# Kernel optimization log

Measured on AMD Instinct MI355X. Metric: run time of the kernel, lower is better.

The kernel has to match this reference:

```python
import jax, jax.numpy as jnp
import numpy as np
from jax import lax

C1, C2 = 64, 128
B, H2, W2 = 16, 64, 64
EPS = 1e-5


def conv2d(x, w, b, pad):
    y = lax.conv_general_dilated(x, w, (1, 1), [(pad, pad), (pad, pad)],
                                 dimension_numbers=('NCHW', 'OIHW', 'NCHW'))
    return y + b[None, :, None, None]


def batchnorm(x, g, be):
    # training-mode BN (batch statistics), matching torch nn.BatchNorm2d default
    m = jnp.mean(x, axis=(0, 2, 3), keepdims=True)
    v = jnp.var(x, axis=(0, 2, 3), keepdims=True)
    return (x - m) * jax.lax.rsqrt(v + EPS) * g[None, :, None, None] + be[None, :, None, None]


def up2_bilinear_ac(x):
    # bilinear upsample x2 with align_corners=True (nn.UpsamplingBilinear2d)
    b, c, h, w = x.shape
    yy = jnp.arange(2 * h, dtype=x.dtype) * ((h - 1) / (2 * h - 1))
    xx = jnp.arange(2 * w, dtype=x.dtype) * ((w - 1) / (2 * w - 1))
    y0 = jnp.floor(yy).astype(jnp.int32); y1 = jnp.minimum(y0 + 1, h - 1)
    x0 = jnp.floor(xx).astype(jnp.int32); x1 = jnp.minimum(x0 + 1, w - 1)
    wy = (yy - y0.astype(x.dtype))
    wx = (xx - x0.astype(x.dtype))
    rows = x[:, :, y0, :] * (1 - wy)[:, None] + x[:, :, y1, :] * wy[:, None]
    return rows[:, :, :, x0] * (1 - wx) + rows[:, :, :, x1] * wx


def dilate(x, k):
    # grayscale morphological dilation with kxk ones kernel == sliding-window max
    return lax.reduce_window(x, -jnp.inf, lax.max, (1, 1, k, k), (1, 1, 1, 1), 'SAME')


def pixel_shuffle2(x):
    b, c, h, w = x.shape
    x = x.reshape(b, c // 4, 2, 2, h, w)
    return x.transpose(0, 1, 4, 2, 5, 3).reshape(b, c // 4, 2 * h, 2 * w)


def setup_inputs() -> dict:
    key = jax.random.key(0)
    ks = jax.random.split(key, 16)
    s = 0.05
    d = {
        'cur_x': jax.random.normal(ks[0], (B, C1, 2 * H2, 2 * W2), jnp.float32),
        'dep_x': jax.random.normal(ks[1], (B, C2, H2, W2), jnp.float32),
        'in_map': jax.random.normal(ks[2], (B, 1, H2, W2), jnp.float32),
        'up_w': jax.random.normal(ks[3], (4 * C1, C2, 3, 3), jnp.float32) * s,
        'up_b': jnp.zeros((4 * C1,), jnp.float32),
        'up_g': jnp.ones((4 * C1,), jnp.float32),
        'up_be': jnp.zeros((4 * C1,), jnp.float32),
        'conv2_w': jax.random.normal(ks[4], (C1, C1, 3, 3), jnp.float32) * s,
        'conv2_b': jnp.zeros((C1,), jnp.float32),
        'beta': jnp.ones((1,), jnp.float32),
        'd1_w': jax.random.normal(ks[5], (C1, C1, 3, 3), jnp.float32) * s,
        'd1_b': jnp.zeros((C1,), jnp.float32),
        'd1_g': jnp.ones((C1,), jnp.float32),
        'd1_be': jnp.zeros((C1,), jnp.float32),
        'd2_w': jax.random.normal(ks[6], (C1, C1, 3, 3), jnp.float32) * s,
        'd2_b': jnp.zeros((C1,), jnp.float32),
        'd2_g': jnp.ones((C1,), jnp.float32),
        'd2_be': jnp.zeros((C1,), jnp.float32),
        'd3_w': jax.random.normal(ks[7], (C1, C1, 3, 3), jnp.float32) * s,
        'd3_b': jnp.zeros((C1,), jnp.float32),
        'd3_g': jnp.ones((C1,), jnp.float32),
        'd3_be': jnp.zeros((C1,), jnp.float32),
        'out_w': jax.random.normal(ks[8], (1, C1, 7, 7), jnp.float32) * s,
        'out_b': jnp.zeros((1,), jnp.float32),
    }
    return d


def reference(cur_x, dep_x, in_map, up_w, up_b, up_g, up_be, conv2_w, conv2_b, beta,
              d1_w, d1_b, d1_g, d1_be, d2_w, d2_b, d2_g, d2_be, d3_w, d3_b, d3_g, d3_be,
              out_w, out_b):
    # up: conv(C2 -> 4*C1) + BN + ReLU, then PixelShuffle(2)
    dep = jax.nn.relu(batchnorm(conv2d(dep_x, up_w, up_b, 1), up_g, up_be))
    dep = pixel_shuffle2(dep)                       # [B, C1, H, W]
    imap = jax.nn.sigmoid(up2_bilinear_ac(in_map))  # [B, 1, H, W]
    # focus_background: dilated(map) - map (increase_input_map is identity, sf=1)
    increase_map = dilate(imap, 3) - imap
    b_feature = cur_x * increase_map
    fn = conv2d(b_feature, conv2_w, conv2_b, 1)
    r = jax.nn.relu(batchnorm(conv2d(dep + beta * fn, d1_w, d1_b, 1), d1_g, d1_be))
    r = jax.nn.relu(batchnorm(conv2d(r, d2_w, d2_b, 1), d2_g, d2_be))
    r = jax.nn.relu(batchnorm(conv2d(r, d3_w, d3_b, 1), d3_g, d3_be))
    output_map = conv2d(r, out_w, out_b, 3)
    return (r, output_map)
```

## Files before the change

### kernel.cpp

```cpp
#include <hip/hip_runtime.h>
#include <hip/hip_bf16.h>

using bf16 = __hip_bfloat16;
typedef __attribute__((ext_vector_type(8))) short bfrag;
typedef __attribute__((ext_vector_type(4))) float ffrag;

__device__ __forceinline__ float b2f(bf16 v) { return __bfloat162float(v); }
__device__ __forceinline__ float ldin(const void* p, int i, int isbf) {
    return isbf ? b2f(((const bf16*)p)[i]) : ((const float*)p)[i];
}
__device__ __forceinline__ void split2(float v, unsigned short& h, unsigned short& l) {
    bf16 hb = __float2bfloat16(v);
    h = __bfloat16_as_ushort(hb);
    l = __bfloat16_as_ushort(__float2bfloat16(v - __bfloat162float(hb)));
}

__global__ void detect_kernel(const unsigned* __restrict__ x, int* __restrict__ flag)
{
    int tid = threadIdx.x;
    int cnt = 0;
    for (int i = tid; i < 256; i += 64) {
        unsigned e = (x[i] >> 7) & 0xFFu;
        cnt += (e >= 110u && e <= 135u) ? 1 : 0;
    }
#pragma unroll
    for (int off = 32; off > 0; off >>= 1) cnt += __shfl_down(cnt, off, 64);
    if (tid == 0) *flag = (cnt >= 128) ? 1 : 0;
}

__global__ void zero_accum_kernel(float* __restrict__ a)
{
    for (int i = threadIdx.x; i < 896; i += 256) a[i] = 0.f;
}

template<int CIN, int COUT>
__global__ __launch_bounds__(256)
void wsplit_kernel(const void* __restrict__ w, unsigned short* __restrict__ whi,
                   unsigned short* __restrict__ wlo, const int* __restrict__ flagp)
{
    constexpr int NCH = CIN / 32, NCOG = COUT / 16;
    constexpr int total = 9 * NCH * NCOG * 512;
    int isbf = *flagp;
    int o = blockIdx.x * 256 + threadIdx.x;
    if (o >= total) return;
    int j = o & 7;
    int l = (o >> 3) & 63;
    int fb = o >> 9;
    int cg = fb % NCOG;
    int t2 = fb / NCOG;
    int ch = t2 % NCH;
    int tap = t2 / NCH;
    int co = cg * 16 + (l & 15);
    int ci = ch * 32 + (l >> 4) * 8 + j;
    float v = ldin(w, (co * CIN + ci) * 9 + tap, isbf);
    unsigned short h, lo2;
    split2(v, h, lo2);
    whi[o] = h;
    wlo[o] = lo2;
}

__global__ __launch_bounds__(256)
void dep_nhwc_kernel(const void* __restrict__ in, unsigned short* __restrict__ outp,
                     const int* __restrict__ flagp)
{
    __shared__ unsigned short s_h[64][65];
    __shared__ unsigned short s_l[64][65];
    const int isbf = *flagp;
    const int pb = blockIdx.x, cb = blockIdx.y, b = blockIdx.z;
    for (int i = threadIdx.x; i < 4096; i += 256) {
        int ci = i >> 6, pi = i & 63;
        float v = ldin(in, ((b * 128 + cb * 64 + ci) << 12) + (pb << 6) + pi, isbf);
        unsigned short h, l;
        split2(v, h, l);
        s_h[ci][pi] = h;
        if (!isbf) s_l[ci][pi] = l;
    }
    __syncthreads();
    for (int i = threadIdx.x; i < 4096; i += 256) {
        int ci = i & 63, pi = i >> 6;
        size_t o = ((size_t)(b * 4096 + pb * 64 + pi) << 7) + cb * 64 + ci;
        outp[o] = s_h[ci][pi];
        if (!isbf) outp[8388608 + o] = s_l[ci][pi];
    }
}

template<int CIN, int COUT, int H, int W, int ROWS, int WCO, int MODE,
         bool SMAP, bool EPI, bool BNIN, bool STATS, int MINW>
__global__ __launch_bounds__(256, MINW)
void conv3_mfma(const void* __restrict__ in,
                const unsigned short* __restrict__ whi,
                const unsigned short* __restrict__ wlo,
                const void* __restrict__ bias,
                const float* __restrict__ imapF,
                const float* __restrict__ dep,
                const void* __restrict__ betap,
                const float* __restrict__ accum,
                const void* __restrict__ bng, const void* __restrict__ bnbe,
                float* __restrict__ out, const int* __restrict__ flagp,
                float* __restrict__ sacc, int statC)
{
    constexpr int NCH  = CIN / 32;
    constexpr int NCOG = COUT / 16;
    constexpr int NCT  = W / 64;
    constexpr int W2h  = 66;
    constexpr int NP   = (ROWS + 2) * W2h;
    constexpr int NPs  = NP + 1;
    constexpr int NE   = 4 * NP;
    constexpr int NF   = (64 / WCO) / 16;
    constexpr int STCO = 64 / WCO;
    constexpr size_t PLANE = (size_t)16 * H * W * CIN;

    __shared__ int4 s_hi[4 * NPs];
    __shared__ int4 s_lo[4 * NPs];
    __shared__ float s_ss[BNIN ? 128 : 1];
    __shared__ float s_sm[SMAP ? NP : 1];
    __shared__ float s_st[STATS ? 2 : 1][4][STCO];

    const int isbf = *flagp;
    const bool uselo = !(isbf && (MODE == 2 || (MODE == 1 && !SMAP)));
    const int tid  = threadIdx.x;
    const int r0   = (blockIdx.x / NCT) * ROWS;
    const int x0   = (blockIdx.x % NCT) * 64;
    const int bimg = r0 / H;
    const int y0im = bimg * H;
    const int coB  = blockIdx.y;

    if (BNIN) {
        if (tid < CIN) {
            const float n = (float)(16 * H * W);
            float S = accum[tid], S2 = accum[CIN + tid];
            float m = S / n;
            float var = fmaxf(S2 / n - m * m, 0.f);
            float scv = ldin(bng, tid, isbf) * rsqrtf(var + 1e-5f);
            s_ss[2 * tid]     = scv;
            s_ss[2 * tid + 1] = ldin(bnbe, tid, isbf) - m * scv;
        }
    }
    if (SMAP) {
        const float* ip = imapF + ((size_t)bimg << 14);
        for (int i = tid; i < NP; i += 256) {
            int rr = i / W2h, cc = i - rr * W2h;
            int gy = r0 - 1 + rr, gx = x0 - 1 + cc;
            float sm = 0.f;
            if (gy >= y0im && gy < y0im + H && (unsigned)gx < (unsigned)W) {
                int y = gy - y0im;
                float ctr = ip[(y << 7) + gx];
                float mx = ctr;
#pragma unroll
                for (int dy = -1; dy <= 1; dy++) {
                    int yy = y + dy;
                    if ((unsigned)yy < 128u) {
#pragma unroll
                        for (int dx = -1; dx <= 1; dx++) {
                            int xx = gx + dx;
                            if ((unsigned)xx < 128u) mx = fmaxf(mx, ip[(yy << 7) + xx]);
                        }
                    }
                }
                sm = mx - ctr;
            }
            s_sm[i] = sm;
        }
    }

    const int lane = tid & 63;
    const int wv = tid >> 6;
    const int wpx = wv / WCO, wco = wv % WCO;
    const int lx = lane & 15;
    const int gq = lane >> 4;

    ffrag acc[4][NF];
#pragma unroll
    for (int mf = 0; mf < 4; mf++)
#pragma unroll
        for (int nf = 0; nf < NF; nf++) acc[mf][nf] = ffrag{0.f, 0.f, 0.f, 0.f};

    for (int ch = 0; ch < NCH; ch++) {
        const int c0 = ch * 32;
        __syncthreads();
        for (int e = tid; e < NE; e += 256) {
            int gg, pixin;
            if (MODE == 1) { gg = e / NP; pixin = e - gg * NP; }
            else           { gg = e & 3;  pixin = e >> 2; }
            int rr = pixin / W2h;
            int cc2 = pixin - rr * W2h;
            int gy = r0 - 1 + rr;
            int gx = x0 - 1 + cc2;
            bool ok = (gy >= y0im) && (gy < y0im + H) && ((unsigned)gx < (unsigned)W);
            if (MODE == 2) {
                int4 hv = make_int4(0, 0, 0, 0), lv = make_int4(0, 0, 0, 0);
                if (ok) {
                    size_t eb = (size_t)(gy * W + gx) * CIN + c0 + 8 * gg;
                    hv = *(const int4*)((const unsigned short*)in + eb);
                    if (!isbf) lv = *(const int4*)((const unsigned short*)in + PLANE + eb);
                }
                s_hi[gg * NPs + pixin] = hv;
                if (!isbf) s_lo[gg * NPs + pixin] = lv;
            } else {
                float v[8];
                if (ok) {
                    if (MODE == 1) {
                        int y = gy - y0im;
                        float sm = SMAP ? s_sm[pixin] : 1.f;
#pragma unroll
                        for (int j = 0; j < 8; j++) {
                            int gi = ((bimg * CIN + c0 + 8 * gg + j) * H + y) * W + gx;
                            v[j] = ldin(in, gi, isbf) * sm;
                        }
                    } else {
                        const float* up = (const float*)in +
                            ((size_t)gy * W + gx) * CIN + c0 + 8 * gg;
                        float4 q0 = *(const float4*)up;
                        float4 q1 = *(const float4*)(up + 4);
                        v[0] = q0.x; v[1] = q0.y; v[2] = q0.z; v[3] = q0.w;
                        v[4] = q1.x; v[5] = q1.y; v[6] = q1.z; v[7] = q1.w;
                        if (BNIN) {
#pragma unroll
                            for (int j = 0; j < 8; j++) {
                                int chn = c0 + 8 * gg + j;
                                v[j] = fmaxf(fmaf(v[j], s_ss[2 * chn], s_ss[2 * chn + 1]), 0.f);
                            }
                        }
                    }
                } else {
#pragma unroll
                    for (int j = 0; j < 8; j++) v[j] = 0.f;
                }
                unsigned hp[4], lp[4];
#pragma unroll
                for (int j2 = 0; j2 < 4; j2++) {
                    bf16 h0b = __float2bfloat16(v[2 * j2]);
                    bf16 h1b = __float2bfloat16(v[2 * j2 + 1]);
                    hp[j2] = (unsigned)__bfloat16_as_ushort(h0b) |
                             ((unsigned)__bfloat16_as_ushort(h1b) << 16);
                    if (uselo) {
                        unsigned short l0 = __bfloat16_as_ushort(
                            __float2bfloat16(v[2 * j2] - b2f(h0b)));
                        unsigned short l1 = __bfloat16_as_ushort(
                            __float2bfloat16(v[2 * j2 + 1] - b2f(h1b)));
                        lp[j2] = (unsigned)l0 | ((unsigned)l1 << 16);
                    }
                }
                s_hi[gg * NPs + pixin] = make_int4(hp[0], hp[1], hp[2], hp[3]);
                if (uselo)
                    s_lo[gg * NPs + pixin] = make_int4(lp[0], lp[1], lp[2], lp[3]);
            }
        }
        __syncthreads();
#pragma unroll
        for (int tap = 0; tap < 9; tap++) {
            const int ky = tap / 3, kx = tap % 3;
            bfrag ah[4];
#pragma unroll
            for (int mf = 0; mf < 4; mf++) {
                int p = 64 * wpx + 16 * mf;
                int rI = (p >> 6) + ky;
                int cI = (p & 63) + kx + lx;
                int pix = rI * W2h + cI;
                ah[mf] = ((const bfrag*)s_hi)[gq * NPs + pix];
            }
            bfrag bh[NF];
#pragma unroll
            for (int nf = 0; nf < NF; nf++) {
                int fb = (tap * NCH + ch) * NCOG + coB * 4 + wco * NF + nf;
                bh[nf] = ((const bfrag*)(whi + (size_t)fb * 512))[lane];
            }
#pragma unroll
            for (int nf = 0; nf < NF; nf++)
#pragma unroll
                for (int mf = 0; mf < 4; mf++)
                    acc[mf][nf] = __builtin_amdgcn_mfma_f32_16x16x32_bf16(
                        ah[mf], bh[nf], acc[mf][nf], 0, 0, 0);
            if (uselo) {
                bfrag al[4];
#pragma unroll
                for (int mf = 0; mf < 4; mf++) {
                    int p = 64 * wpx + 16 * mf;
                    int rI = (p >> 6) + ky;
                    int cI = (p & 63) + kx + lx;
                    int pix = rI * W2h + cI;
                    al[mf] = ((const bfrag*)s_lo)[gq * NPs + pix];
                }
#pragma unroll
                for (int nf = 0; nf < NF; nf++)
#pragma unroll
                    for (int mf = 0; mf < 4; mf++)
                        acc[mf][nf] = __builtin_amdgcn_mfma_f32_16x16x32_bf16(
                            al[mf], bh[nf], acc[mf][nf], 0, 0, 0);
            }
            if (!isbf) {
                bfrag ah2[4];
#pragma unroll
                for (int mf = 0; mf < 4; mf++) {
                    int p = 64 * wpx + 16 * mf;
                    int rI = (p >> 6) + ky;
                    int cI = (p & 63) + kx + lx;
                    int pix = rI * W2h + cI;
                    ah2[mf] = ((const bfrag*)s_hi)[gq * NPs + pix];
                }
                bfrag bl[NF];
#pragma unroll
                for (int nf = 0; nf < NF; nf++) {
                    int fb = (tap * NCH + ch) * NCOG + coB * 4 + wco * NF + nf;
                    bl[nf] = ((const bfrag*)(wlo + (size_t)fb * 512))[lane];
                }
#pragma unroll
                for (int nf = 0; nf < NF; nf++)
#pragma unroll
                    for (int mf = 0; mf < 4; mf++)
                        acc[mf][nf] = __builtin_amdgcn_mfma_f32_16x16x32_bf16(
                            ah2[mf], bl[nf], acc[mf][nf], 0, 0, 0);
            }
        }
    }
    const float beta = EPI ? ldin(betap, 0, isbf) : 0.f;
    float sl[NF], s2l[NF];
#pragma unroll
    for (int nf = 0; nf < NF; nf++) { sl[nf] = 0.f; s2l[nf] = 0.f; }
#pragma unroll
    for (int nf = 0; nf < NF; nf++) {
        int co = coB * 64 + wco * STCO + nf * 16 + lx;
        float bi = ldin(bias, co, isbf);
#pragma unroll
        for (int mf = 0; mf < 4; mf++) {
#pragma unroll
            for (int r2 = 0; r2 < 4; r2++) {
                int p = 64 * wpx + 16 * mf + gq * 4 + r2;
                int grow = r0 + (p >> 6);
                int gcol = x0 + (p & 63);
                size_t oi = ((size_t)grow * W + gcol) * COUT + co;
                float vo = acc[mf][nf][r2] + bi;
                if (EPI) vo = dep[oi] + beta * vo;
                out[oi] = vo;
                if (STATS) {
                    sl[nf] += vo;
                    s2l[nf] = fmaf(vo, vo, s2l[nf]);
                }
            }
        }
    }
    if (STATS) {
#pragma unroll
        for (int nf = 0; nf < NF; nf++) {
            float s = sl[nf], q = s2l[nf];
            s += __shfl_xor(s, 16, 64); s += __shfl_xor(s, 32, 64);
            q += __shfl_xor(q, 16, 64); q += __shfl_xor(q, 32, 64);
            if (gq == 0) {
                s_st[0][wv][nf * 16 + lx] = s;
                s_st[1][wv][nf * 16 + lx] = q;
            }
        }
        __syncthreads();
        if (tid < 128) {
            int which = tid >> 6, c = tid & 63;
            float v;
            if (WCO == 1) {
                v = s_st[which][0][c] + s_st[which][1][c] +
                    s_st[which][2][c] + s_st[which][3][c];
            } else {
                int wc = c >> 5, ci = c & 31;
                v = s_st[which][wc][ci] + s_st[which][2 + wc][ci];
            }
            atomicAdd(&sacc[which * statC + coB * 64 + c], v);
        }
    }
}

__global__ __launch_bounds__(256)
void shuffle_bn_nhwc_kernel(const float* __restrict__ u, const float* __restrict__ accum,
                            const void* __restrict__ g, const void* __restrict__ be,
                            float* __restrict__ dep, const int* __restrict__ flagp)
{
    int isbf = *flagp;
    int tid = threadIdx.x;
    int c = tid & 63, ps = tid >> 6;
    float sc[4], sh[4];
#pragma unroll
    for (int q = 0; q < 4; q++) {
        int chn = 4 * c + q;
        float S = accum[chn], S2 = accum[256 + chn];
        const float n = 65536.f;
        float m = S / n;
        float var = fmaxf(S2 / n - m * m, 0.f);
        sc[q] = ldin(g, chn, isbf) * rsqrtf(var + 1e-5f);
        sh[q] = ldin(be, chn, isbf) - m * sc[q];
    }
    for (int sp = blockIdx.x * 4 + ps; sp < 65536; sp += gridDim.x * 4) {
        float4 q4 = *(const float4*)(u + (size_t)sp * 256 + 4 * c);
        float vals[4] = {q4.x, q4.y, q4.z, q4.w};
        int b = sp >> 12, rem = sp & 4095, y2 = rem >> 6, x2 = rem & 63;
#pragma unroll
        for (int dy = 0; dy < 2; dy++)
#pragma unroll
            for (int dx = 0; dx < 2; dx++) {
                int q = 2 * dy + dx;
                float v = fmaxf(fmaf(vals[q], sc[q], sh[q]), 0.f);
                size_t op = (size_t)(b * 128 + 2 * y2 + dy) * 128 + (2 * x2 + dx);
                dep[op * 64 + c] = v;
            }
    }
}

__global__ __launch_bounds__(256)
void imap_kernel(const void* __restrict__ im, float* __restrict__ imap,
                 const int* __restrict__ flagp)
{
    int isbf = *flagp;
    int idx = blockIdx.x * 256 + threadIdx.x;
    int x = idx & 127, y = (idx >> 7) & 127, b = idx >> 14;
    const float s = (float)(63.0 / 127.0);
    float yy = y * s, xx = x * s;
    int y0 = (int)yy, x0 = (int)xx;
    float wy = yy - y0, wx = xx - x0;
    int y1 = min(y0 + 1, 63), x1 = min(x0 + 1, 63);
    int base = b << 12;
    float v00 = ldin(im, base + (y0 << 6) + x0, isbf);
    float v01 = ldin(im, base + (y0 << 6) + x1, isbf);
    float v10 = ldin(im, base + (y1 << 6) + x0, isbf);
    float v11 = ldin(im, base + (y1 << 6) + x1, isbf);
    float r0 = v00 * (1.f - wy) + v10 * wy;
    float r1 = v01 * (1.f - wy) + v11 * wy;
    float v = r0 * (1.f - wx) + r1 * wx;
    imap[idx] = 1.f / (1.f + expf(-v));
}

__global__ __launch_bounds__(256)
void bn_out_kernel(const float* __restrict__ u, const float* __restrict__ accum,
                   const void* __restrict__ g, const void* __restrict__ be,
                   float* __restrict__ r3, void* __restrict__ dout,
                   const int* __restrict__ flagp)
{
    int isbf = *flagp;
    int tid = threadIdx.x;
    int c = tid & 63, ps = tid >> 6;
    float S = accum[c], S2 = accum[64 + c];
    const float n = 262144.f;
    float m = S / n;
    float var = fmaxf(S2 / n - m * m, 0.f);
    float sc = ldin(g, c, isbf) * rsqrtf(var + 1e-5f);
    float sh = ldin(be, c, isbf) - m * sc;
    __shared__ float s[64][65];
    int pix0 = blockIdx.x * 64;
#pragma unroll
    for (int ii = 0; ii < 16; ii++) {
        int p = ps + 4 * ii;
        float v = u[(size_t)(pix0 + p) * 64 + c];
        s[p][c] = fmaxf(fmaf(v, sc, sh), 0.f);
    }
    __syncthreads();
    int x = c;
    int row = pix0 >> 7, col0 = pix0 & 127;
    int b = row >> 7, y = row & 127;
#pragma unroll
    for (int jj = 0; jj < 16; jj++) {
        int cc = ps + 4 * jj;
        float v = s[x][cc];
        size_t oi = (((size_t)(b * 64 + cc)) << 14) + (y << 7) + col0 + x;
        r3[oi] = v;
        if (isbf) ((bf16*)dout)[oi] = __float2bfloat16(v);
        else      ((float*)dout)[oi] = v;
    }
}

__global__ __launch_bounds__(256, 2)
void conv7x7_part_kernel(const float* __restrict__ r, const void* __restrict__ w,
                         float* __restrict__ outP, const int* __restrict__ flagp)
{
    __shared__ float s_in[4][70][22];
    __shared__ float s_w[16][49];
    const int isbf = *flagp;
    int tid = threadIdx.x;
    int tx = tid & 15, ty = tid >> 4;
    int x0 = blockIdx.x * 16, y0 = blockIdx.y * 64;
    int b = blockIdx.z >> 2, g = blockIdx.z & 3;
    for (int i = tid; i < 16 * 49; i += 256) {
        int ci = i / 49, k = i - ci * 49;
        s_w[ci][k] = ldin(w, (g * 16 + ci) * 49 + k, isbf);
    }
    float acc[4] = {0.f, 0.f, 0.f, 0.f};

    for (int c0 = 0; c0 < 16; c0 += 4) {
        __syncthreads();
        for (int i = tid; i < 4 * 70 * 22; i += 256) {
            int ci = i / (70 * 22);
            int rem = i - ci * (70 * 22);
            int rr = rem / 22, cc = rem - rr * 22;
            int gy = y0 + rr - 3, gx = x0 + cc - 3;
            float v = 0.f;
            if ((unsigned)gy < 128u && (unsigned)gx < 128u)
                v = r[((b * 64 + g * 16 + c0 + ci) << 14) + (gy << 7) + gx];
            s_in[ci][rr][cc] = v;
        }
        __syncthreads();
        for (int ci = 0; ci < 4; ci++) {
            float wr[49];
#pragma unroll
            for (int k = 0; k < 49; k++) wr[k] = s_w[c0 + ci][k];
#pragma unroll
            for (int rr = 0; rr < 10; rr++) {
                float row[7];
#pragma unroll
                for (int c = 0; c < 7; c++) row[c] = s_in[ci][4 * ty + rr][tx + c];
#pragma unroll
                for (int oy = 0; oy < 4; oy++) {
                    int ky = rr - oy;
                    if (ky >= 0 && ky <= 6) {
#pragma unroll
                        for (int kx = 0; kx < 7; kx++)
                            acc[oy] = fmaf(row[kx], wr[ky * 7 + kx], acc[oy]);
                    }
                }
            }
        }
    }
#pragma unroll
    for (int oy = 0; oy < 4; oy++) {
        int y = y0 + 4 * ty + oy;
        outP[(g << 18) + (b << 14) + (y << 7) + x0 + tx] = acc[oy];
    }
}

__global__ __launch_bounds__(256)
void finalize_out_kernel(const float* __restrict__ outP, const void* __restrict__ bias,
                         void* __restrict__ outv, const int* __restrict__ flagp)
{
    int isbf = *flagp;
    int i = blockIdx.x * 256 + threadIdx.x;
    float bi = ldin(bias, 0, isbf);
    float v = (outP[i] + outP[i + 262144]) +
              (outP[i + 2 * 262144] + outP[i + 3 * 262144]) + bi;
    int oidx = 16777216 + i;
    if (isbf) ((bf16*)outv)[oidx] = __float2bfloat16(v);
    else      ((float*)outv)[oidx] = v;
}

extern "C" void kernel_launch(void* const* d_in, const int* in_sizes, int n_in,
                              void* d_out, int out_size, void* d_ws, size_t ws_size,
                              hipStream_t stream)
{
    (void)in_sizes; (void)n_in; (void)out_size; (void)ws_size;

    const void* cur_x   = d_in[0];
    const void* dep_x   = d_in[1];
    const void* in_map  = d_in[2];
    const void* up_w    = d_in[3];
    const void* up_b    = d_in[4];
    const void* up_g    = d_in[5];
    const void* up_be   = d_in[6];
    const void* conv2_w = d_in[7];
    const void* conv2_b = d_in[8];
    const void* beta    = d_in[9];
    const void* d1_w = d_in[10];
    const void* d1_b = d_in[11];
    const void* d1_g = d_in[12];
    const void* d1_be = d_in[13];
    const void* d2_w = d_in[14];
    const void* d2_b = d_in[15];
    const void* d2_g = d_in[16];
    const void* d2_be = d_in[17];
    const void* d3_w = d_in[18];
    const void* d3_b = d_in[19];
    const void* d3_g = d_in[20];
    const void* d3_be = d_in[21];
    const void* out_w = d_in[22];
    const void* out_b = d_in[23];

    char* ws = (char*)d_ws;
    float* W0    = (float*)ws;
    float* W1    = (float*)(ws + 67108864);
    float* accum = (float*)(ws + 134217728);
    int*   flag  = (int*)(ws + 134221824);
    float* a0 = accum;
    float* a1 = accum + 512;
    float* a2 = accum + 640;
    float* a3 = accum + 768;

    char* sc = (char*)d_out;
    unsigned short* whi1  = (unsigned short*)sc;
    unsigned short* wlo1  = whi1 + 294912;
    unsigned short* whi2  = wlo1 + 294912;
    unsigned short* wlo2  = whi2 + 36864;
    unsigned short* whiD1 = wlo2 + 36864;
    unsigned short* wloD1 = whiD1 + 36864;
    unsigned short* whiD2 = wloD1 + 36864;
    unsigned short* wloD2 = whiD2 + 36864;
    unsigned short* whiD3 = wloD2 + 36864;
    unsigned short* wloD3 = whiD3 + 36864;
    float* imapF = (float*)(sc + 1769472);

    detect_kernel<<<1, 64, 0, stream>>>((const unsigned*)cur_x, flag);
    zero_accum_kernel<<<1, 256, 0, stream>>>(accum);
    wsplit_kernel<128, 256><<<1152, 256, 0, stream>>>(up_w, whi1, wlo1, flag);
    wsplit_kernel<64, 64><<<144, 256, 0, stream>>>(conv2_w, whi2, wlo2, flag);
    wsplit_kernel<64, 64><<<144, 256, 0, stream>>>(d1_w, whiD1, wloD1, flag);
    wsplit_kernel<64, 64><<<144, 256, 0, stream>>>(d2_w, whiD2, wloD2, flag);
    wsplit_kernel<64, 64><<<144, 256, 0, stream>>>(d3_w, whiD3, wloD3, flag);
    dep_nhwc_kernel<<<dim3(64, 2, 16), 256, 0, stream>>>(
        dep_x, (unsigned short*)W1, flag);

    conv3_mfma<128, 256, 64, 64, 4, 1, 2, false, false, false, true, 3>
        <<<dim3(256, 4), 256, 0, stream>>>((const void*)W1, whi1, wlo1, up_b,
            nullptr, nullptr, nullptr, nullptr, nullptr, nullptr, W0, flag, a0, 256);
    imap_kernel<<<1024, 256, 0, stream>>>(in_map, imapF, flag);
    shuffle_bn_nhwc_kernel<<<2048, 256, 0, stream>>>(W0, a0, up_g, up_be, W1, flag);
    conv3_mfma<64, 64, 128, 128, 2, 2, 1, true, true, false, false, 4>
        <<<dim3(2048, 1), 256, 0, stream>>>(cur_x, whi2, wlo2, conv2_b,
            imapF, W1, beta, nullptr, nullptr, nullptr, W0, flag, nullptr, 0);
    conv3_mfma<64, 64, 128, 128, 2, 2, 0, false, false, false, true, 4>
        <<<dim3(2048, 1), 256, 0, stream>>>(W0, whiD1, wloD1, d1_b,
            nullptr, nullptr, nullptr, nullptr, nullptr, nullptr, W1, flag, a1, 64);
    conv3_mfma<64, 64, 128, 128, 2, 2, 0, false, false, true, true, 4>
        <<<dim3(2048, 1), 256, 0, stream>>>(W1, whiD2, wloD2, d2_b,
            nullptr, nullptr, nullptr, a1, d1_g, d1_be, W0, flag, a2, 64);
    conv3_mfma<64, 64, 128, 128, 2, 2, 0, false, false, true, true, 4>
        <<<dim3(2048, 1), 256, 0, stream>>>(W0, whiD3, wloD3, d3_b,
            nullptr, nullptr, nullptr, a2, d2_g, d2_be, W1, flag, a3, 64);
    bn_out_kernel<<<4096, 256, 0, stream>>>(W1, a3, d3_g, d3_be, W0, d_out, flag);
    conv7x7_part_kernel<<<dim3(8, 2, 64), 256, 0, stream>>>(W0, out_w, W1, flag);
    finalize_out_kernel<<<1024, 256, 0, stream>>>(W1, out_b, d_out, flag);
}
```

Baseline: 798.1 us.

## Merge prep kernels and specialize up-conv by dtype to shrink LDS

Folds dtype detection, accumulator zeroing and all five weight-split launches into a single prep kernel, cutting six small launches. The first conv is now launched twice with a compile-time dtype mode. Each variant returns early unless the runtime flag matches, and the bf16 variant drops the low-part LDS buffer so it can target higher occupancy (launch bound 6). The stats scratch now aliases the s_hi buffer, with an added barrier to keep that safe. This adds one extra empty launch per call and a small risk around the aliasing.

New measurement: 786.4 us. Within noise of the previous version (-1.5%).

```diff
diff --git a/kernel.cpp b/kernel.cpp
--- a/kernel.cpp
+++ b/kernel.cpp
@@ -15,37 +15,50 @@
     l = __bfloat16_as_ushort(__float2bfloat16(v - __bfloat162float(hb)));
 }
 
-__global__ void detect_kernel(const unsigned* __restrict__ x, int* __restrict__ flag)
-{
-    int tid = threadIdx.x;
-    int cnt = 0;
-    for (int i = tid; i < 256; i += 64) {
-        unsigned e = (x[i] >> 7) & 0xFFu;
-        cnt += (e >= 110u && e <= 135u) ? 1 : 0;
-    }
-#pragma unroll
-    for (int off = 32; off > 0; off >>= 1) cnt += __shfl_down(cnt, off, 64);
-    if (tid == 0) *flag = (cnt >= 128) ? 1 : 0;
-}
-
-__global__ void zero_accum_kernel(float* __restrict__ a)
-{
-    for (int i = threadIdx.x; i < 896; i += 256) a[i] = 0.f;
-}
-
-template<int CIN, int COUT>
 __global__ __launch_bounds__(256)
-void wsplit_kernel(const void* __restrict__ w, unsigned short* __restrict__ whi,
-                   unsigned short* __restrict__ wlo, const int* __restrict__ flagp)
-{
-    constexpr int NCH = CIN / 32, NCOG = COUT / 16;
-    constexpr int total = 9 * NCH * NCOG * 512;
-    int isbf = *flagp;
-    int o = blockIdx.x * 256 + threadIdx.x;
-    if (o >= total) return;
-    int j = o & 7;
-    int l = (o >> 3) & 63;
-    int fb = o >> 9;
+void prep_kernel(const unsigned* __restrict__ cur_x,
+                 const void* __restrict__ up_w, const void* __restrict__ c2_w,
+                 const void* __restrict__ d1_w, const void* __restrict__ d2_w,
+                 const void* __restrict__ d3_w,
+                 unsigned short* __restrict__ wbase,
+                 float* __restrict__ accum, int* __restrict__ flagout)
+{
+    __shared__ int s_flag;
+    const int tid = threadIdx.x;
+    if (tid < 64) {
+        int cnt = 0;
+        for (int i = tid; i < 256; i += 64) {
+            unsigned e = (cur_x[i] >> 7) & 0xFFu;
+            cnt += (e >= 110u && e <= 135u) ? 1 : 0;
+        }
+#pragma unroll
+        for (int off = 32; off > 0; off >>= 1) cnt += __shfl_down(cnt, off, 64);
+        if (tid == 0) s_flag = (cnt >= 128) ? 1 : 0;
+    }
+    __syncthreads();
+    const int isbf = s_flag;
+    if (blockIdx.x == 0) {
+        if (tid == 0) *flagout = isbf;
+        for (int i = tid; i < 896; i += 256) accum[i] = 0.f;
+    }
+    int o = blockIdx.x * 256 + tid;
+    if (o >= 442368) return;
+    const void* w;
+    int CIN, NCH, NCOG, lo;
+    size_t hoff, losz;
+    if (o < 294912) {
+        w = up_w; CIN = 128; NCH = 4; NCOG = 16; hoff = 0; lo = o; losz = 294912;
+    } else {
+        int t = (o - 294912) / 36864;
+        lo = (o - 294912) - t * 36864;
+        CIN = 64; NCH = 2; NCOG = 4;
+        hoff = 589824 + (size_t)t * 73728;
+        losz = 36864;
+        w = (t == 0) ? c2_w : (t == 1) ? d1_w : (t == 2) ? d2_w : d3_w;
+    }
+    int j = lo & 7;
+    int l = (lo >> 3) & 63;
+    int fb = lo >> 9;
     int cg = fb % NCOG;
     int t2 = fb / NCOG;
     int ch = t2 % NCH;
@@ -53,10 +66,10 @@
     int co = cg * 16 + (l & 15);
     int ci = ch * 32 + (l >> 4) * 8 + j;
     float v = ldin(w, (co * CIN + ci) * 9 + tap, isbf);
-    unsigned short h, lo2;
-    split2(v, h, lo2);
-    whi[o] = h;
-    wlo[o] = lo2;
+    unsigned short h, l2;
+    split2(v, h, l2);
+    wbase[hoff + lo] = h;
+    wbase[hoff + losz + lo] = l2;
 }
 
 __global__ __launch_bounds__(256)
@@ -85,7 +98,7 @@
 }
 
 template<int CIN, int COUT, int H, int W, int ROWS, int WCO, int MODE,
-         bool SMAP, bool EPI, bool BNIN, bool STATS, int MINW>
+         bool SMAP, bool EPI, bool BNIN, bool STATS, int MINW, int DTMODE = -1>
 __global__ __launch_bounds__(256, MINW)
 void conv3_mfma(const void* __restrict__ in,
                 const unsigned short* __restrict__ whi,
@@ -109,14 +122,17 @@
     constexpr int NF   = (64 / WCO) / 16;
     constexpr int STCO = 64 / WCO;
     constexpr size_t PLANE = (size_t)16 * H * W * CIN;
+    constexpr bool NOLO = (DTMODE == 1) && (MODE == 2) && !SMAP;
+
+    if (DTMODE >= 0 && *flagp != DTMODE) return;
+    const int isbf = (DTMODE >= 0) ? DTMODE : *flagp;
 
     __shared__ int4 s_hi[4 * NPs];
-    __shared__ int4 s_lo[4 * NPs];
+    __shared__ int4 s_lo[NOLO ? 1 : 4 * NPs];
     __shared__ float s_ss[BNIN ? 128 : 1];
     __shared__ float s_sm[SMAP ? NP : 1];
-    __shared__ float s_st[STATS ? 2 : 1][4][STCO];
-
-    const int isbf = *flagp;
+    float (*s_st)[4][STCO] = (float (*)[4][STCO])s_hi;
+
     const bool uselo = !(isbf && (MODE == 2 || (MODE == 1 && !SMAP)));
     const int tid  = threadIdx.x;
     const int r0   = (blockIdx.x / NCT) * ROWS;
@@ -195,7 +211,7 @@
                     if (!isbf) lv = *(const int4*)((const unsigned short*)in + PLANE + eb);
                 }
                 s_hi[gg * NPs + pixin] = hv;
-                if (!isbf) s_lo[gg * NPs + pixin] = lv;
+                if (!isbf && !NOLO) s_lo[gg * NPs + pixin] = lv;
             } else {
                 float v[8];
                 if (ok) {
@@ -242,7 +258,7 @@
                     }
                 }
                 s_hi[gg * NPs + pixin] = make_int4(hp[0], hp[1], hp[2], hp[3]);
-                if (uselo)
+                if (uselo && !NOLO)
                     s_lo[gg * NPs + pixin] = make_int4(lp[0], lp[1], lp[2], lp[3]);
             }
         }
@@ -271,7 +287,7 @@
                 for (int mf = 0; mf < 4; mf++)
                     acc[mf][nf] = __builtin_amdgcn_mfma_f32_16x16x32_bf16(
                         ah[mf], bh[nf], acc[mf][nf], 0, 0, 0);
-            if (uselo) {
+            if (!NOLO && uselo) {
                 bfrag al[4];
 #pragma unroll
                 for (int mf = 0; mf < 4; mf++) {
@@ -340,6 +356,7 @@
         }
     }
     if (STATS) {
+        __syncthreads();
 #pragma unroll
         for (int nf = 0; nf < NF; nf++) {
             float s = sl[nf], q = s2l[nf];
@@ -576,7 +593,8 @@
     float* a3 = accum + 768;
 
     char* sc = (char*)d_out;
-    unsigned short* whi1  = (unsigned short*)sc;
+    unsigned short* wbase = (unsigned short*)sc;
+    unsigned short* whi1  = wbase;
     unsigned short* wlo1  = whi1 + 294912;
     unsigned short* whi2  = wlo1 + 294912;
     unsigned short* wlo2  = whi2 + 36864;
@@ -588,17 +606,15 @@
     unsigned short* wloD3 = whiD3 + 36864;
     float* imapF = (float*)(sc + 1769472);
 
-    detect_kernel<<<1, 64, 0, stream>>>((const unsigned*)cur_x, flag);
-    zero_accum_kernel<<<1, 256, 0, stream>>>(accum);
-    wsplit_kernel<128, 256><<<1152, 256, 0, stream>>>(up_w, whi1, wlo1, flag);
-    wsplit_kernel<64, 64><<<144, 256, 0, stream>>>(conv2_w, whi2, wlo2, flag);
-    wsplit_kernel<64, 64><<<144, 256, 0, stream>>>(d1_w, whiD1, wloD1, flag);
-    wsplit_kernel<64, 64><<<144, 256, 0, stream>>>(d2_w, whiD2, wloD2, flag);
-    wsplit_kernel<64, 64><<<144, 256, 0, stream>>>(d3_w, whiD3, wloD3, flag);
+    prep_kernel<<<1728, 256, 0, stream>>>((const unsigned*)cur_x,
+        up_w, conv2_w, d1_w, d2_w, d3_w, wbase, accum, flag);
     dep_nhwc_kernel<<<dim3(64, 2, 16), 256, 0, stream>>>(
         dep_x, (unsigned short*)W1, flag);
 
-    conv3_mfma<128, 256, 64, 64, 4, 1, 2, false, false, false, true, 3>
+    conv3_mfma<128, 256, 64, 64, 4, 1, 2, false, false, false, true, 6, 1>
+        <<<dim3(256, 4), 256, 0, stream>>>((const void*)W1, whi1, wlo1, up_b,
+            nullptr, nullptr, nullptr, nullptr, nullptr, nullptr, W0, flag, a0, 256);
+    conv3_mfma<128, 256, 64, 64, 4, 1, 2, false, false, false, true, 3, 0>
         <<<dim3(256, 4), 256, 0, stream>>>((const void*)W1, whi1, wlo1, up_b,
             nullptr, nullptr, nullptr, nullptr, nullptr, nullptr, W0, flag, a0, 256);
     imap_kernel<<<1024, 256, 0, stream>>>(in_map, imapF, flag);
```
